# Optimization experiments

Hardware: AMD Instinct MI355X
Metric: run time of the kernel (lower is better)

The kernel has to match this reference:

```python
import jax, jax.numpy as jnp
import numpy as np

N = 16000   # query points
M = 16000   # support points
NB = 32     # neighbors per query
A = 4       # kanchor (SO(2)/z-axis discrete anchors, kanchor<10 branch)
K = 15      # kernel points
CIN = 32
COUT = 32
RADIUS = 1.0
KP_EXTENT = 0.6


def _make_kernel_points(key):
    # KPConv-style kernel points inside a sphere of radius 0.66*RADIUS, first point at center
    kp = jax.random.normal(key, (K, 3), dtype=jnp.float32)
    kp = kp / (jnp.linalg.norm(kp, axis=-1, keepdims=True) + 1e-8)
    r = jax.random.uniform(jax.random.fold_in(key, 1), (K, 1), dtype=jnp.float32) ** (1.0 / 3.0)
    kp = kp * r * (0.66 * RADIUS)
    return kp.at[0].set(0.0)


def _make_anchors():
    # kanchor=4 -> rotations about z by 2*pi*a/A (E2PN get_anchors for kanchor<10)
    ang = 2.0 * jnp.pi * jnp.arange(A, dtype=jnp.float32) / A
    c, s = jnp.cos(ang), jnp.sin(ang)
    z = jnp.zeros_like(c)
    o = jnp.ones_like(c)
    return jnp.stack([c, -s, z, s, c, z, z, z, o], axis=-1).reshape(A, 3, 3)


def setup_inputs() -> dict:
    key = jax.random.key(0)
    k1, k2, k3, k4, k5, k6 = jax.random.split(key, 6)
    q_pts = jax.random.uniform(k1, (N, 3), dtype=jnp.float32) * 0.5
    s_pts = jax.random.uniform(k2, (M, 3), dtype=jnp.float32) * 0.5
    neighb_inds = jax.random.randint(k3, (N, NB), 0, M, dtype=jnp.int32)
    x = jax.random.normal(k4, (M, A, CIN), dtype=jnp.float32)
    kernel_points = _make_kernel_points(k5)
    anchors = _make_anchors()
    # kaiming-uniform-ish init of the (K, C_in, C_out) separable conv weights
    bound = float(np.sqrt(6.0 / ((1 + 5) * CIN)))
    weights = jax.random.uniform(k6, (K, CIN, COUT), dtype=jnp.float32,
                                 minval=-bound, maxval=bound)
    return {"q_pts": q_pts, "s_pts": s_pts, "neighb_inds": neighb_inds, "x": x,
            "kernel_points": kernel_points, "anchors": anchors, "weights": weights}


def reference(q_pts, s_pts, neighb_inds, x, kernel_points, anchors, weights):
    # neighbor gather, centered on query points: [N, NB, 3]
    neighbors = s_pts[neighb_inds] - q_pts[:, None, :]
    # rotate kernel points by each anchor: [A, K, 3]
    rot_kp = jnp.einsum('aij,kj->aki', anchors, kernel_points)
    # squared distances via |n|^2 + |kp|^2 - 2 n.kp (avoids [A,N,NB,K,3] blowup)
    n2 = jnp.sum(neighbors * neighbors, axis=-1)          # [N, NB]
    k2 = jnp.sum(rot_kp * rot_kp, axis=-1)                # [A, K]
    cross = jnp.einsum('nbj,akj->anbk', neighbors, rot_kp)
    sq_distances = n2[None, :, :, None] + k2[:, None, None, :] - 2.0 * cross  # [A,N,NB,K]
    # linear KP influence, clamped at 0
    all_weights = jnp.clip(1.0 - jnp.sqrt(jnp.maximum(sq_distances, 1e-12)) / KP_EXTENT,
                           0.0, None)                      # [A, N, NB, K]
    # gather neighbor features: [N, NB, A, C_in]
    neighb_x = x[neighb_inds]
    # weight neighbors onto kernel points (sum aggregation): [A, N, K, C_in]
    weighted_feats = jnp.einsum('anbk,nbac->ankc', all_weights, neighb_x)
    # per-kernel-point small GEMMs, summed over K: [N, A, C_out]
    out = jnp.einsum('ankc,kcd->nad', weighted_feats, weights)
    return out
```

## Files before the change

kernel.cpp:

```cpp
#include <hip/hip_runtime.h>


typedef short bf16x8 __attribute__((ext_vector_type(8)));
typedef float f32x4  __attribute__((ext_vector_type(4)));

__device__ __forceinline__ unsigned short f2bf(float f) {
    unsigned u = __builtin_bit_cast(unsigned, f);
    return (unsigned short)((u + 0x8000u) >> 16);
}

__device__ __forceinline__ unsigned pack2bf(float hi, float lo) {
    unsigned uh = __builtin_bit_cast(unsigned, hi) + 0x8000u;
    unsigned ul = __builtin_bit_cast(unsigned, lo) + 0x8000u;
    return __builtin_amdgcn_perm(uh, ul, 0x07060302u);
}

__global__ void prep_kernel(const float* __restrict__ W, unsigned short* __restrict__ Wp) {
    const int idx = blockIdx.x * 256 + threadIdx.x;
    const int kk = idx >> 10, d = (idx >> 5) & 31, e = idx & 31;
    const int kcs = kk * 32 + e;
    const int c = kcs >> 4, k = kcs & 15;
    const float v = (k < 15) ? W[(k * 32 + c) * 32 + d] : 0.0f;
    Wp[idx] = f2bf(v);
}

__global__ __launch_bounds__(256) void kpconv_mfma(
    const float* __restrict__ q_pts,
    const float* __restrict__ s_pts,
    const int*   __restrict__ inds,
    const float* __restrict__ x,
    const float* __restrict__ kp,
    const float* __restrict__ anchors,
    const unsigned short* __restrict__ Wp,
    float*       __restrict__ out)
{
    __shared__ __align__(16) unsigned short xa_s[16384];
    __shared__ __align__(16) float nbr[576];
    __shared__ __align__(16) float rk_s[256];
    __shared__ int sidx[128];

    const int t  = threadIdx.x;
    const int n0 = blockIdx.x * 4;

    if (t < 128) {
        const int q = t >> 5, b = t & 31;
        const int idx = inds[(n0 + q) * 32 + b];
        sidx[t] = idx;
        const float qx = q_pts[(n0 + q) * 3 + 0];
        const float qy = q_pts[(n0 + q) * 3 + 1];
        const float qz = q_pts[(n0 + q) * 3 + 2];
        const float nx = s_pts[idx * 3 + 0] - qx;
        const float ny = s_pts[idx * 3 + 1] - qy;
        const float nz = s_pts[idx * 3 + 2] - qz;
        float4 v; v.x = nx; v.y = ny; v.z = nz; v.w = nx*nx + ny*ny + nz*nz;
        *(float4*)&nbr[(q * 36 + b + (b >> 3)) * 4] = v;
    } else if (t < 192) {
        const int j = t - 128;
        const int a = j >> 4, k = j & 15;
        float4 v;
        if (k < 15) {
            const float kx = kp[k*3+0], ky = kp[k*3+1], kz = kp[k*3+2];
            const float* R = anchors + a * 9;
            v.x = R[0]*kx + R[1]*ky + R[2]*kz;
            v.y = R[3]*kx + R[4]*ky + R[5]*kz;
            v.z = R[6]*kx + R[7]*ky + R[8]*kz;
            v.w = v.x*v.x + v.y*v.y + v.z*v.z;
        } else {
            v.x = 0.0f; v.y = 0.0f; v.z = 0.0f; v.w = 1e30f;
        }
        *(float4*)&rk_s[(a * 16 + k) * 4] = v;
    }
    __syncthreads();

    {
        const int c4 = t & 7, bg = (t >> 3) & 7, q = t >> 6;
        #pragma unroll
        for (int a = 0; a < 4; ++a) {
            float4 v[4];
            #pragma unroll
            for (int i = 0; i < 4; ++i) {
                const int row = sidx[q * 32 + 4 * bg + i];
                v[i] = ((const float4*)x)[row * 32 + a * 8 + c4];
            }
            const float* vp = (const float*)v;
            #pragma unroll
            for (int j = 0; j < 4; ++j) {
                const int c  = 4 * c4 + j;
                const int fc = c4 & 3;
                const int bb = 4 * (bg & 1) + 8 * ((bg >> 1) ^ fc);
                uint2 w;
                w.x = pack2bf(vp[1 * 4 + j], vp[0 * 4 + j]);
                w.y = pack2bf(vp[3 * 4 + j], vp[2 * 4 + j]);
                *(uint2*)&xa_s[((a * 4 + q) * 32 + c) * 32 + bb] = w;
            }
        }
    }
    __syncthreads();

    const int a    = t >> 6;
    const int lane = t & 63;
    const int l15  = lane & 15;
    const int quad = lane >> 4;
    const int fc   = (l15 >> 2) & 3;

    const float4 r4 = *(const float4*)&rk_s[(a * 16 + l15) * 4];
    unsigned short* wfb = &xa_s[a * 4096];

    #pragma unroll
    for (int q = 0; q < 4; ++q) {
        float w8[8];
        #pragma unroll
        for (int j = 0; j < 8; ++j) {
            const int b = quad * 8 + j;
            const float4 nb = *(const float4*)&nbr[(q * 36 + b + (b >> 3)) * 4];
            const float dot = fmaf(nb.x, r4.x, fmaf(nb.y, r4.y, nb.z * r4.z));
            const float sq  = fmaf(-2.0f, dot, nb.w + r4.w);
            const float d   = sqrtf(fmaxf(sq, 1e-12f));
            w8[j] = fmaxf(fmaf(d, -(1.0f / 0.6f), 1.0f), 0.0f);
        }
        uint4 uu;
        uu.x = pack2bf(w8[1], w8[0]); uu.y = pack2bf(w8[3], w8[2]);
        uu.z = pack2bf(w8[5], w8[4]); uu.w = pack2bf(w8[7], w8[6]);
        const bf16x8 afr = __builtin_bit_cast(bf16x8, uu);

        const bf16x8 b0 = *(const bf16x8*)&xa_s[((a*4 + q)*32 + l15)      * 32 + 8 * (quad ^ fc)];
        const bf16x8 b1 = *(const bf16x8*)&xa_s[((a*4 + q)*32 + l15 + 16) * 32 + 8 * (quad ^ fc)];
        f32x4 d0 = {0.f,0.f,0.f,0.f}, d1 = {0.f,0.f,0.f,0.f};
        d0 = __builtin_amdgcn_mfma_f32_16x16x32_bf16(afr, b0, d0, 0, 0, 0);
        d1 = __builtin_amdgcn_mfma_f32_16x16x32_bf16(afr, b1, d1, 0, 0, 0);
        uint2 s0, s1;
        s0.x = pack2bf(d0[1], d0[0]); s0.y = pack2bf(d0[3], d0[2]);
        s1.x = pack2bf(d1[1], d1[0]); s1.y = pack2bf(d1[3], d1[2]);
        *(uint2*)&wfb[q*512 + (( l15       * 16 + quad * 4) ^ (q * 16))] = s0;
        *(uint2*)&wfb[q*512 + (((l15 + 16) * 16 + quad * 4) ^ (q * 16))] = s1;
    }

    const int qq = l15 & 3;
    f32x4 o0 = {0.f,0.f,0.f,0.f}, o1 = {0.f,0.f,0.f,0.f};
    #pragma unroll
    for (int kk = 0; kk < 16; ++kk) {
        const bf16x8 a2 = *(const bf16x8*)&wfb[qq*512 + ((kk*32 + quad*8) ^ (qq*16))];
        const bf16x8 w0 = *(const bf16x8*)&Wp[kk*1024 + l15*32 + quad*8];
        const bf16x8 w1 = *(const bf16x8*)&Wp[kk*1024 + (l15+16)*32 + quad*8];
        o0 = __builtin_amdgcn_mfma_f32_16x16x32_bf16(a2, w0, o0, 0, 0, 0);
        o1 = __builtin_amdgcn_mfma_f32_16x16x32_bf16(a2, w1, o1, 0, 0, 0);
    }
    if (quad == 0) {
        #pragma unroll
        for (int r = 0; r < 4; ++r) {
            out[((n0 + r) * 4 + a) * 32 + l15]      = o0[r];
            out[((n0 + r) * 4 + a) * 32 + 16 + l15] = o1[r];
        }
    }
}

extern "C" void kernel_launch(void* const* d_in, const int* in_sizes, int n_in,
                              void* d_out, int out_size, void* d_ws, size_t ws_size,
                              hipStream_t stream) {
    const float* q_pts   = (const float*)d_in[0];
    const float* s_pts   = (const float*)d_in[1];
    const int*   inds    = (const int*)d_in[2];
    const float* x       = (const float*)d_in[3];
    const float* kp      = (const float*)d_in[4];
    const float* anchors = (const float*)d_in[5];
    const float* weights = (const float*)d_in[6];
    float*       out     = (float*)d_out;
    unsigned short* Wp   = (unsigned short*)d_ws;

    prep_kernel<<<dim3(64), dim3(256), 0, stream>>>(weights, Wp);
    kpconv_mfma<<<dim3(4000), dim3(256), 0, stream>>>(
        q_pts, s_pts, inds, x, kp, anchors, Wp, out);
}
```

Measured before the change: 122.7 us.

## Pre-convert features to bf16 and gather them without the index sync

Adds a prep kernel that converts the whole feature tensor x to bf16 in workspace once per call. The main kernel then gathers half-width rows, loading neighbor indices straight from global memory instead of staging them in shared memory. This removes one __syncthreads and halves the bytes moved by the random gather. The cost is an extra full pass over x (read fp32, write bf16) and one more kernel launch.

```diff
diff --git a/kernel.cpp b/kernel.cpp
--- a/kernel.cpp
+++ b/kernel.cpp
@@ -15,7 +15,7 @@
     return __builtin_amdgcn_perm(uh, ul, 0x07060302u);
 }
 
-__global__ void prep_kernel(const float* __restrict__ W, unsigned short* __restrict__ Wp) {
+__global__ void prep_w(const float* __restrict__ W, unsigned short* __restrict__ Wp) {
     const int idx = blockIdx.x * 256 + threadIdx.x;
     const int kk = idx >> 10, d = (idx >> 5) & 31, e = idx & 31;
     const int kcs = kk * 32 + e;
@@ -24,11 +24,21 @@
     Wp[idx] = f2bf(v);
 }
 
+__global__ void prep_x(const float* __restrict__ x, unsigned short* __restrict__ xb) {
+    const int i = (blockIdx.x * 256 + threadIdx.x) * 8;
+    const float4 v0 = *(const float4*)&x[i];
+    const float4 v1 = *(const float4*)&x[i + 4];
+    uint4 u;
+    u.x = pack2bf(v0.y, v0.x); u.y = pack2bf(v0.w, v0.z);
+    u.z = pack2bf(v1.y, v1.x); u.w = pack2bf(v1.w, v1.z);
+    *(uint4*)&xb[i] = u;
+}
+
 __global__ __launch_bounds__(256) void kpconv_mfma(
     const float* __restrict__ q_pts,
     const float* __restrict__ s_pts,
     const int*   __restrict__ inds,
-    const float* __restrict__ x,
+    const unsigned short* __restrict__ xb,
     const float* __restrict__ kp,
     const float* __restrict__ anchors,
     const unsigned short* __restrict__ Wp,
@@ -37,15 +47,43 @@
     __shared__ __align__(16) unsigned short xa_s[16384];
     __shared__ __align__(16) float nbr[576];
     __shared__ __align__(16) float rk_s[256];
-    __shared__ int sidx[128];
 
     const int t  = threadIdx.x;
     const int n0 = blockIdx.x * 4;
 
+    {
+        const int c4 = t & 7, bg = (t >> 3) & 7, q = t >> 6;
+        const int4 rows = *(const int4*)&inds[(n0 + q) * 32 + 4 * bg];
+        const int fc  = c4 & 3;
+        const int bb  = 4 * (bg & 1);
+        const int blk = 8 * ((bg >> 1) ^ fc);
+        unsigned short* base = &xa_s[(q * 32) * 32 + blk + bb];
+        #pragma unroll
+        for (int a = 0; a < 4; ++a) {
+            const uint2 r0 = *(const uint2*)&xb[rows.x * 128 + a * 32 + c4 * 4];
+            const uint2 r1 = *(const uint2*)&xb[rows.y * 128 + a * 32 + c4 * 4];
+            const uint2 r2 = *(const uint2*)&xb[rows.z * 128 + a * 32 + c4 * 4];
+            const uint2 r3 = *(const uint2*)&xb[rows.w * 128 + a * 32 + c4 * 4];
+            unsigned short* pa = base + a * 4096;
+            uint2 w;
+            w.x = __builtin_amdgcn_perm(r1.x, r0.x, 0x05040100u);
+            w.y = __builtin_amdgcn_perm(r3.x, r2.x, 0x05040100u);
+            *(uint2*)&pa[(4 * c4 + 0) * 32] = w;
+            w.x = __builtin_amdgcn_perm(r1.x, r0.x, 0x07060302u);
+            w.y = __builtin_amdgcn_perm(r3.x, r2.x, 0x07060302u);
+            *(uint2*)&pa[(4 * c4 + 1) * 32] = w;
+            w.x = __builtin_amdgcn_perm(r1.y, r0.y, 0x05040100u);
+            w.y = __builtin_amdgcn_perm(r3.y, r2.y, 0x05040100u);
+            *(uint2*)&pa[(4 * c4 + 2) * 32] = w;
+            w.x = __builtin_amdgcn_perm(r1.y, r0.y, 0x07060302u);
+            w.y = __builtin_amdgcn_perm(r3.y, r2.y, 0x07060302u);
+            *(uint2*)&pa[(4 * c4 + 3) * 32] = w;
+        }
+    }
+
     if (t < 128) {
         const int q = t >> 5, b = t & 31;
         const int idx = inds[(n0 + q) * 32 + b];
-        sidx[t] = idx;
         const float qx = q_pts[(n0 + q) * 3 + 0];
         const float qy = q_pts[(n0 + q) * 3 + 1];
         const float qz = q_pts[(n0 + q) * 3 + 2];
@@ -69,31 +107,6 @@
             v.x = 0.0f; v.y = 0.0f; v.z = 0.0f; v.w = 1e30f;
         }
         *(float4*)&rk_s[(a * 16 + k) * 4] = v;
-    }
-    __syncthreads();
-
-    {
-        const int c4 = t & 7, bg = (t >> 3) & 7, q = t >> 6;
-        #pragma unroll
-        for (int a = 0; a < 4; ++a) {
-            float4 v[4];
-            #pragma unroll
-            for (int i = 0; i < 4; ++i) {
-                const int row = sidx[q * 32 + 4 * bg + i];
-                v[i] = ((const float4*)x)[row * 32 + a * 8 + c4];
-            }
-            const float* vp = (const float*)v;
-            #pragma unroll
-            for (int j = 0; j < 4; ++j) {
-                const int c  = 4 * c4 + j;
-                const int fc = c4 & 3;
-                const int bb = 4 * (bg & 1) + 8 * ((bg >> 1) ^ fc);
-                uint2 w;
-                w.x = pack2bf(vp[1 * 4 + j], vp[0 * 4 + j]);
-                w.y = pack2bf(vp[3 * 4 + j], vp[2 * 4 + j]);
-                *(uint2*)&xa_s[((a * 4 + q) * 32 + c) * 32 + bb] = w;
-            }
-        }
     }
     __syncthreads();
 
@@ -165,9 +178,12 @@
     const float* anchors = (const float*)d_in[5];
     const float* weights = (const float*)d_in[6];
     float*       out     = (float*)d_out;
-    unsigned short* Wp   = (unsigned short*)d_ws;
 
-    prep_kernel<<<dim3(64), dim3(256), 0, stream>>>(weights, Wp);
+    unsigned short* Wp = (unsigned short*)d_ws;
+    unsigned short* xb = (unsigned short*)((char*)d_ws + (1 << 16));
+
+    prep_w<<<dim3(64),   dim3(256), 0, stream>>>(weights, Wp);
+    prep_x<<<dim3(1000), dim3(256), 0, stream>>>(x, xb);
     kpconv_mfma<<<dim3(4000), dim3(256), 0, stream>>>(
-        q_pts, s_pts, inds, x, kp, anchors, Wp, out);
+        q_pts, s_pts, inds, xb, kp, anchors, Wp, out);
 }
```

After: 123.8 us. Within noise of the previous version (+0.9%).
